# Kernel tuning notes

Measured on AMD Instinct MI355X. Metric: run time of the kernel, lower is better.

The kernel has to match this reference:

```python
import jax, jax.numpy as jnp
import numpy as np

N, F_IN, H1, NHEADS, H2, H3 = 4096, 512, 128, 4, 256, 64
ALPHA = 0.2
NEG = -9e15


def setup_inputs() -> dict:
    key = jax.random.key(0)
    k_x, k_adj, k_watt, k_a, k_w1, k_w2 = jax.random.split(key, 6)
    x = jax.random.normal(k_x, (N, F_IN), dtype=jnp.float32)
    adj = (jax.random.uniform(k_adj, (N, N)) < 0.004).astype(jnp.float32)
    adj = adj.at[jnp.arange(N), jnp.arange(N)].set(1.0)
    # xavier-ish init scales
    W_att = jax.random.normal(k_watt, (NHEADS, F_IN, H1), dtype=jnp.float32) * (1.0 / np.sqrt(F_IN))
    a = jax.random.normal(k_a, (NHEADS, 2 * H1), dtype=jnp.float32) * 0.1
    W1 = jax.random.normal(k_w1, (NHEADS * H1, H2), dtype=jnp.float32) * (1.0 / np.sqrt(NHEADS * H1))
    W2 = jax.random.normal(k_w2, (H2, H3), dtype=jnp.float32) * (1.0 / np.sqrt(H2))
    return {"x": x, "adj": adj, "W_att": W_att, "a": a, "W1": W1, "W2": W2}


def reference(x, adj, W_att, a, W1, W2):
    h1 = W_att.shape[-1]
    # --- multi-head GAT (dense masked attention, faithful to source) ---
    Wh = jnp.einsum('nf,hfo->hno', x, W_att)              # [H, N, h1]
    a1, a2 = a[:, :h1], a[:, h1:]                          # each [H, h1]
    s1 = jnp.einsum('hno,ho->hn', Wh, a1)                  # [H, N]
    s2 = jnp.einsum('hno,ho->hn', Wh, a2)                  # [H, N]
    e = jax.nn.leaky_relu(s1[:, :, None] + s2[:, None, :], ALPHA)  # [H, N, N]
    att = jax.nn.softmax(jnp.where(adj[None] > 0, e, NEG), axis=-1)
    h = jnp.einsum('hnm,hmo->hno', att, Wh)                # [H, N, h1]
    xcat = jnp.transpose(h, (1, 0, 2)).reshape(x.shape[0], -1)  # [N, H*h1]
    xr = jax.nn.relu(xcat)
    # --- GCN layers: support = x @ W; out = adj @ support ---
    g1 = jax.nn.relu(adj @ (xr @ W1))                      # [N, H2]
    g2 = adj @ (g1 @ W2)                                   # [N, H3]
    return g2, jax.nn.softmax(g2, axis=1)
```

## Files before the change

kernel.cpp:

```cpp
#include <hip/hip_runtime.h>
#include <hip/hip_bf16.h>

#define NN    4096
#define FIN   512
#define NH1   128
#define NH    4
#define NH2   256
#define NH3   64
#define CAP   64
#define ALPHA 0.2f

typedef float f32x4 __attribute__((ext_vector_type(4)));
typedef __bf16 bf16x8 __attribute__((ext_vector_type(8)));

__device__ __forceinline__ unsigned short f2bf(float f) {
    union { float f; unsigned u; } x; x.f = f;
    unsigned r = x.u + 0x7fff + ((x.u >> 16) & 1);
    return (unsigned short)(r >> 16);
}
__device__ __forceinline__ float bf2f(ushort u) {
    union { unsigned u; float f; } x; x.u = ((unsigned)u) << 16;
    return x.f;
}
__device__ __forceinline__ float bflo(unsigned w) {
    union { unsigned u; float f; } x; x.u = w << 16; return x.f;
}
__device__ __forceinline__ float bfhi(unsigned w) {
    union { unsigned u; float f; } x; x.u = w & 0xffff0000u; return x.f;
}

#define C_X     2048
#define C_WATT  (C_X + 1024)
#define C_W1T   (C_WATT + 512)
#define C_W2B   (C_W1T + 16)
#define C_Z     (C_W2B + 32)

__global__ __launch_bounds__(256) void k_conv(
    const float* __restrict__ x, ushort* __restrict__ xb,
    const float* __restrict__ W_att, ushort* __restrict__ Wattb,
    const float* __restrict__ W1, ushort* __restrict__ W1t,
    const float* __restrict__ W2, ushort* __restrict__ W2b,
    float* __restrict__ s1s2) {
    int bid = blockIdx.x;
    int tid = threadIdx.x;
    if (bid < C_X) {
        int i = (bid * 256 + tid) * 4;
        float4 v = *reinterpret_cast<const float4*>(x + i);
        ushort4 o;
        o.x = f2bf(v.x); o.y = f2bf(v.y); o.z = f2bf(v.z); o.w = f2bf(v.w);
        *reinterpret_cast<ushort4*>(xb + i) = o;
    } else if (bid < C_WATT) {
        int idx = (bid - C_X) * 256 + tid;
        int col = idx >> 9, f = idx & 511;
        int h = col >> 7, o = col & 127;
        Wattb[idx] = f2bf(W_att[h * (FIN * NH1) + f * NH1 + o]);
    } else if (bid < C_W1T) {
        int idx = (bid - C_WATT) * 256 + tid;
        int c = idx >> 9, r = idx & 511;
        W1t[idx] = f2bf(W1[(size_t)r * NH2 + c]);
    } else if (bid < C_W2B) {
        int i = ((bid - C_W1T) * 256 + tid) * 4;
        float4 v = *reinterpret_cast<const float4*>(W2 + i);
        ushort4 o;
        o.x = f2bf(v.x); o.y = f2bf(v.y); o.z = f2bf(v.z); o.w = f2bf(v.w);
        *reinterpret_cast<ushort4*>(W2b + i) = o;
    } else {
        int i = (bid - C_W2B) * 256 + tid;
        f32x4 z = {0.f, 0.f, 0.f, 0.f};
        *reinterpret_cast<f32x4*>(s1s2 + i * 4) = z;
    }
}

template <int SCORES, int MT, int BYBITS>
__global__ __launch_bounds__(256) void k_gemm(const ushort* __restrict__ A,
                                              const ushort* __restrict__ Bt,
                                              ushort* __restrict__ Cb,
                                              const float* __restrict__ av,
                                              float* __restrict__ s1,
                                              float* __restrict__ s2,
                                              int M, int N, int K) {
    __shared__ ushort As[2][32 * MT * 64];
    __shared__ ushort Bs[2][64 * 64];
    const int tid = threadIdx.x;
    const int wid = tid >> 6;
    const int lane = tid & 63;
    const int bid = blockIdx.x;
    const int row0 = (bid & ((1 << BYBITS) - 1)) * (32 * MT);
    const int col0 = (bid >> BYBITS) * 64;
    const int wr = wid >> 1, wc = wid & 1;

    f32x4 acc[MT][2] = {};
    const int nt = K / 64;

    auto stage = [&](int buf, int k0) {
        #pragma unroll
        for (int j = 0; j < MT; ++j) {
            int ci = j * 256 + tid;
            int r = ci >> 3;
            int sc = (ci & 7) ^ (r & 7);
            const ushort* ga = A + (size_t)(row0 + r) * K + k0 + sc * 8;
            ushort* la = &As[buf][(size_t)ci * 8];
            __builtin_amdgcn_global_load_lds(
                (const __attribute__((address_space(1))) unsigned int*)ga,
                (__attribute__((address_space(3))) unsigned int*)la, 16, 0, 0);
        }
        #pragma unroll
        for (int j = 0; j < 2; ++j) {
            int ci = j * 256 + tid;
            int r = ci >> 3;
            int sc = (ci & 7) ^ (r & 7);
            const ushort* gb = Bt + (size_t)(col0 + r) * K + k0 + sc * 8;
            ushort* lb = &Bs[buf][(size_t)ci * 8];
            __builtin_amdgcn_global_load_lds(
                (const __attribute__((address_space(1))) unsigned int*)gb,
                (__attribute__((address_space(3))) unsigned int*)lb, 16, 0, 0);
        }
    };

    stage(0, 0);
    __syncthreads();
    int cur = 0;
    for (int t = 0; t < nt; ++t) {
        if (t + 1 < nt) stage(cur ^ 1, (t + 1) * 64);
        #pragma unroll
        for (int kk = 0; kk < 2; ++kk) {
            bf16x8 af[MT], bfv[2];
            #pragma unroll
            for (int m = 0; m < MT; ++m) {
                int r = wr * (16 * MT) + m * 16 + (lane & 15);
                int kc = kk * 4 + (lane >> 4);
                int off = r * 64 + (((kc ^ (r & 7)) & 7) << 3);
                af[m] = *reinterpret_cast<const bf16x8*>(&As[cur][off]);
            }
            #pragma unroll
            for (int n = 0; n < 2; ++n) {
                int c = wc * 32 + n * 16 + (lane & 15);
                int kc = kk * 4 + (lane >> 4);
                int off = c * 64 + (((kc ^ (c & 7)) & 7) << 3);
                bfv[n] = *reinterpret_cast<const bf16x8*>(&Bs[cur][off]);
            }
            #pragma unroll
            for (int m = 0; m < MT; ++m)
                #pragma unroll
                for (int n = 0; n < 2; ++n)
                    acc[m][n] = __builtin_amdgcn_mfma_f32_16x16x32_bf16(af[m], bfv[n], acc[m][n], 0, 0, 0);
        }
        __syncthreads();
        cur ^= 1;
    }
    #pragma unroll
    for (int m = 0; m < MT; ++m)
        #pragma unroll
        for (int n = 0; n < 2; ++n) {
            int col = col0 + wc * 32 + n * 16 + (lane & 15);
            #pragma unroll
            for (int j2 = 0; j2 < 4; ++j2) {
                int row = row0 + wr * (16 * MT) + m * 16 + (lane >> 4) * 4 + j2;
                Cb[(size_t)row * N + col] = f2bf(acc[m][n][j2]);
            }
        }
    if (SCORES) {
        int h = col0 >> 7;
        float a1v[2], a2v[2];
        #pragma unroll
        for (int n = 0; n < 2; ++n) {
            int colh = (col0 & 127) + wc * 32 + n * 16 + (lane & 15);
            a1v[n] = av[h * 256 + colh];
            a2v[n] = av[h * 256 + 128 + colh];
        }
        #pragma unroll
        for (int m = 0; m < MT; ++m)
            #pragma unroll
            for (int j2 = 0; j2 < 4; ++j2) {
                float v1 = acc[m][0][j2] * a1v[0] + acc[m][1][j2] * a1v[1];
                float v2 = acc[m][0][j2] * a2v[0] + acc[m][1][j2] * a2v[1];
                #pragma unroll
                for (int off = 1; off < 16; off <<= 1) {
                    v1 += __shfl_xor(v1, off);
                    v2 += __shfl_xor(v2, off);
                }
                if ((lane & 15) == 0) {
                    int row = row0 + wr * (16 * MT) + m * 16 + (lane >> 4) * 4 + j2;
                    atomicAdd(&s1[h * NN + row], v1);
                    atomicAdd(&s2[h * NN + row], v2);
                }
            }
    }
}

__global__ __launch_bounds__(256) void k_attn_csr(const float* __restrict__ adj,
                                                  const ushort* __restrict__ Whb,
                                                  const float* __restrict__ s1,
                                                  const float* __restrict__ s2,
                                                  int* __restrict__ nbr,
                                                  int* __restrict__ cnt,
                                                  ushort* __restrict__ xrb) {
    __shared__ int lds_list[4][64];
    __shared__ int lds_cnt[4];
    __shared__ int mlist[CAP];
    __shared__ int stot;
    int n = blockIdx.x;
    int tid = threadIdx.x;
    int wid = tid >> 6;
    int lane = tid & 63;

    const uint4* arow = (const uint4*)(adj + (size_t)n * NN);
    uint4 v[4];
    #pragma unroll
    for (int it = 0; it < 4; ++it) v[it] = arow[wid * 256 + it * 64 + lane];
    const unsigned long long below = (1ull << lane) - 1ull;
    int base = 0;
    #pragma unroll
    for (int it = 0; it < 4; ++it) {
        unsigned long long b0 = __ballot(v[it].x != 0u);
        unsigned long long b1 = __ballot(v[it].y != 0u);
        unsigned long long b2 = __ballot(v[it].z != 0u);
        unsigned long long b3 = __ballot(v[it].w != 0u);
        int pre = __popcll(b0 & below) + __popcll(b1 & below) +
                  __popcll(b2 & below) + __popcll(b3 & below);
        int col0 = wid * 1024 + it * 256 + lane * 4;
        int pos = base + pre;
        if (v[it].x != 0u) { if (pos < 64) lds_list[wid][pos] = col0;     ++pos; }
        if (v[it].y != 0u) { if (pos < 64) lds_list[wid][pos] = col0 + 1; ++pos; }
        if (v[it].z != 0u) { if (pos < 64) lds_list[wid][pos] = col0 + 2; ++pos; }
        if (v[it].w != 0u) { if (pos < 64) lds_list[wid][pos] = col0 + 3; ++pos; }
        base += __popcll(b0) + __popcll(b1) + __popcll(b2) + __popcll(b3);
    }
    if (lane == 0) lds_cnt[wid] = base;
    __syncthreads();
    int c0 = lds_cnt[0], c1 = lds_cnt[1], c2 = lds_cnt[2], c3 = lds_cnt[3];
    {
        int off = (wid > 0 ? c0 : 0) + (wid > 1 ? c1 : 0) + (wid > 2 ? c2 : 0);
        int my = lds_cnt[wid]; if (my > 64) my = 64;
        if (lane < my) {
            int gpos = off + lane;
            if (gpos < CAP) {
                mlist[gpos] = lds_list[wid][lane];
                nbr[n * CAP + gpos] = lds_list[wid][lane];
            }
        }
        if (tid == 0) {
            int tot = c0 + c1 + c2 + c3;
            stot = tot < CAP ? tot : CAP;
            cnt[n] = stot;
        }
    }
    __syncthreads();
    int c = stot;

    int h = wid;
    int m = mlist[lane < c ? lane : 0];
    float e = -1e30f;
    float s1n = s1[h * NN + n];
    if (lane < c) {
        float t = s1n + s2[h * NN + m];
        e = (t >= 0.0f) ? t : ALPHA * t;
    }
    float mx = e;
    #pragma unroll
    for (int off = 32; off; off >>= 1) mx = fmaxf(mx, __shfl_xor(mx, off));
    float p = (lane < c) ? __expf(e - mx) : 0.0f;
    float s = p;
    #pragma unroll
    for (int off = 32; off; off >>= 1) s += __shfl_xor(s, off);
    p /= s;
    const ushort* wb = Whb + h * 128 + 2 * lane;
    float acc0 = 0.0f, acc1 = 0.0f;
    int cp8 = (c + 7) & ~7;
    for (int j = 0; j < cp8; j += 8) {
        float pj[8]; int mj[8]; unsigned wj[8];
        #pragma unroll
        for (int u = 0; u < 8; ++u) {
            pj[u] = __shfl(p, j + u);
            mj[u] = __shfl(m, j + u);
        }
        #pragma unroll
        for (int u = 0; u < 8; ++u)
            wj[u] = *reinterpret_cast<const unsigned*>(wb + (size_t)mj[u] * 512);
        #pragma unroll
        for (int u = 0; u < 8; ++u) {
            acc0 = fmaf(pj[u], bflo(wj[u]), acc0);
            acc1 = fmaf(pj[u], bfhi(wj[u]), acc1);
        }
    }
    unsigned ow = (unsigned)f2bf(fmaxf(acc0, 0.0f)) | ((unsigned)f2bf(fmaxf(acc1, 0.0f)) << 16);
    *reinterpret_cast<unsigned*>(xrb + (size_t)n * 512 + h * 128 + 2 * lane) = ow;
}

__global__ __launch_bounds__(256) void k_g1y2(const ushort* __restrict__ y1b,
                                              const int* __restrict__ nbr,
                                              const int* __restrict__ cnt,
                                              const ushort* __restrict__ W2b,
                                              float* __restrict__ y2) {
    __shared__ float g1s[2][NH2];
    __shared__ float part[2][2][NH3];
    int half = threadIdx.x >> 7;
    int t = threadIdx.x & 127;
    int n = blockIdx.x * 2 + half;
    int c = cnt[n];
    const int* nb = nbr + n * CAP;
    {
        float acc0 = 0.0f, acc1 = 0.0f;
        const ushort* yb = y1b + 2 * t;
        for (int j = 0; j < c; j += 8) {
            int idx[8]; float f[8]; unsigned w[8];
            #pragma unroll
            for (int u = 0; u < 8; ++u) {
                idx[u] = nb[(j + u < c) ? j + u : j];
                f[u] = (j + u < c) ? 1.f : 0.f;
            }
            #pragma unroll
            for (int u = 0; u < 8; ++u)
                w[u] = *reinterpret_cast<const unsigned*>(yb + (size_t)idx[u] * NH2);
            #pragma unroll
            for (int u = 0; u < 8; ++u) {
                acc0 = fmaf(f[u], bflo(w[u]), acc0);
                acc1 = fmaf(f[u], bfhi(w[u]), acc1);
            }
        }
        g1s[half][2 * t]     = fmaxf(acc0, 0.0f);
        g1s[half][2 * t + 1] = fmaxf(acc1, 0.0f);
    }
    __syncthreads();
    int q = t >> 6, col = t & 63;
    float acc = 0.0f;
    #pragma unroll 8
    for (int i = 0; i < 128; ++i) {
        int k = q * 128 + i;
        acc = fmaf(g1s[half][k], bf2f(W2b[k * NH3 + col]), acc);
    }
    part[half][q][col] = acc;
    __syncthreads();
    if (t < 64)
        y2[(size_t)n * NH3 + t] = part[half][0][t] + part[half][1][t];
}

__global__ __launch_bounds__(256) void k_final(const float* __restrict__ Y2,
                                               const int* __restrict__ nbr,
                                               const int* __restrict__ cnt,
                                               float* __restrict__ out) {
    int n = blockIdx.x * 4 + (threadIdx.x >> 6);
    int lane = threadIdx.x & 63;
    int c = cnt[n];
    const int* nb = nbr + n * CAP;
    float acc = 0.0f;
    for (int j = 0; j < c; j += 8) {
        int idx[8]; float f[8]; float v[8];
        #pragma unroll
        for (int u = 0; u < 8; ++u) {
            idx[u] = nb[(j + u < c) ? j + u : j];
            f[u] = (j + u < c) ? 1.f : 0.f;
        }
        #pragma unroll
        for (int u = 0; u < 8; ++u)
            v[u] = Y2[(size_t)idx[u] * NH3 + lane];
        #pragma unroll
        for (int u = 0; u < 8; ++u)
            acc = fmaf(f[u], v[u], acc);
    }
    out[(size_t)n * NH3 + lane] = acc;
    float mx = acc;
    #pragma unroll
    for (int off = 32; off; off >>= 1) mx = fmaxf(mx, __shfl_xor(mx, off));
    float p = __expf(acc - mx);
    float s = p;
    #pragma unroll
    for (int off = 32; off; off >>= 1) s += __shfl_xor(s, off);
    out[(size_t)NN * NH3 + (size_t)n * NH3 + lane] = p / s;
}

extern "C" void kernel_launch(void* const* d_in, const int* in_sizes, int n_in,
                              void* d_out, int out_size, void* d_ws, size_t ws_size,
                              hipStream_t stream) {
    const float* x     = (const float*)d_in[0];
    const float* adj   = (const float*)d_in[1];
    const float* W_att = (const float*)d_in[2];
    const float* a     = (const float*)d_in[3];
    const float* W1    = (const float*)d_in[4];
    const float* W2    = (const float*)d_in[5];
    float* out = (float*)d_out;

    char* p = (char*)d_ws;
    ushort* xb    = (ushort*)p; p += (size_t)NN * FIN * 2;
    ushort* Wattb = (ushort*)p; p += (size_t)FIN * NH * NH1 * 2;
    ushort* W1t   = (ushort*)p; p += (size_t)NH2 * (NH * NH1) * 2;
    ushort* W2b   = (ushort*)p; p += (size_t)NH2 * NH3 * 2;
    ushort* Whb   = (ushort*)p; p += (size_t)NN * NH * NH1 * 2;
    float*  s1    = (float*)p;  p += (size_t)NH * NN * 4;
    float*  s2    = (float*)p;  p += (size_t)NH * NN * 4;
    int*    nbr   = (int*)p;    p += (size_t)NN * CAP * 4;
    int*    cnt   = (int*)p;    p += (size_t)NN * 4;
    ushort* xrb   = (ushort*)p; p += (size_t)NN * NH * NH1 * 2;
    ushort* y1b   = (ushort*)p; p += (size_t)NN * NH2 * 2;
    float*  y2    = (float*)p;  p += (size_t)NN * NH3 * 4;

    k_conv<<<C_Z, 256, 0, stream>>>(x, xb, W_att, Wattb, W1, W1t, W2, W2b, s1);
    k_gemm<1, 2, 6><<<512, 256, 0, stream>>>(
        xb, Wattb, Whb, a, s1, s2, NN, NH * NH1, FIN);
    k_attn_csr<<<NN, 256, 0, stream>>>(adj, Whb, s1, s2, nbr, cnt, xrb);
    k_gemm<0, 1, 7><<<512, 256, 0, stream>>>(
        xrb, W1t, y1b, nullptr, nullptr, nullptr, NN, NH2, NH * NH1);
    k_g1y2<<<NN / 2, 256, 0, stream>>>(y1b, nbr, cnt, W2b, y2);
    k_final<<<NN / 4, 256, 0, stream>>>(y2, nbr, cnt, out);
}
```

Before: 66.21 us.

## Reassociate second GCN layer and move weight conversion into attention kernel

Computes adj@(g1@W2) as (adj@g1)@W2. The neighbor aggregation now runs on the 256-wide g1 (stored as bf16), and the 256x64 projection is fused into the final kernel together with the softmax. The W1/W2 bf16 conversions move from the first conversion kernel into extra blocks of the attention launch, so they no longer sit in front of the first GEMM. In exchange, the second gather is wider (256 bf16 instead of 64 fp32 per neighbor), g1 is rounded to bf16 before aggregation, and only two of four waves do the projection.

```diff
diff --git a/kernel.cpp b/kernel.cpp
--- a/kernel.cpp
+++ b/kernel.cpp
@@ -30,16 +30,14 @@
 }
 
 #define C_X     2048
+#define C_WATT  (C_X + 512)
+#undef C_WATT
 #define C_WATT  (C_X + 1024)
-#define C_W1T   (C_WATT + 512)
-#define C_W2B   (C_W1T + 16)
-#define C_Z     (C_W2B + 32)
+#define C_Z     (C_WATT + 32)
 
 __global__ __launch_bounds__(256) void k_conv(
     const float* __restrict__ x, ushort* __restrict__ xb,
     const float* __restrict__ W_att, ushort* __restrict__ Wattb,
-    const float* __restrict__ W1, ushort* __restrict__ W1t,
-    const float* __restrict__ W2, ushort* __restrict__ W2b,
     float* __restrict__ s1s2) {
     int bid = blockIdx.x;
     int tid = threadIdx.x;
@@ -54,18 +52,8 @@
         int col = idx >> 9, f = idx & 511;
         int h = col >> 7, o = col & 127;
         Wattb[idx] = f2bf(W_att[h * (FIN * NH1) + f * NH1 + o]);
-    } else if (bid < C_W1T) {
-        int idx = (bid - C_WATT) * 256 + tid;
-        int c = idx >> 9, r = idx & 511;
-        W1t[idx] = f2bf(W1[(size_t)r * NH2 + c]);
-    } else if (bid < C_W2B) {
-        int i = ((bid - C_W1T) * 256 + tid) * 4;
-        float4 v = *reinterpret_cast<const float4*>(W2 + i);
-        ushort4 o;
-        o.x = f2bf(v.x); o.y = f2bf(v.y); o.z = f2bf(v.z); o.w = f2bf(v.w);
-        *reinterpret_cast<ushort4*>(W2b + i) = o;
     } else {
-        int i = (bid - C_W2B) * 256 + tid;
+        int i = (bid - C_WATT) * 256 + tid;
         f32x4 z = {0.f, 0.f, 0.f, 0.f};
         *reinterpret_cast<f32x4*>(s1s2 + i * 4) = z;
     }
@@ -188,19 +176,42 @@
     }
 }
 
+#define ATT_N   4096
+#define ATT_W1  (ATT_N + 512)
+#define ATT_W2  (ATT_W1 + 16)
+
 __global__ __launch_bounds__(256) void k_attn_csr(const float* __restrict__ adj,
                                                   const ushort* __restrict__ Whb,
                                                   const float* __restrict__ s1,
                                                   const float* __restrict__ s2,
                                                   int* __restrict__ nbr,
                                                   int* __restrict__ cnt,
-                                                  ushort* __restrict__ xrb) {
+                                                  ushort* __restrict__ xrb,
+                                                  const float* __restrict__ W1,
+                                                  ushort* __restrict__ W1t,
+                                                  const float* __restrict__ W2,
+                                                  ushort* __restrict__ W2b) {
+    int tid = threadIdx.x;
+    if (blockIdx.x >= ATT_N) {
+        int bid = blockIdx.x;
+        if (bid < ATT_W1) {
+            int idx = (bid - ATT_N) * 256 + tid;
+            int c = idx >> 9, r = idx & 511;
+            W1t[idx] = f2bf(W1[(size_t)r * NH2 + c]);
+        } else {
+            int i = ((bid - ATT_W1) * 256 + tid) * 4;
+            float4 v = *reinterpret_cast<const float4*>(W2 + i);
+            ushort4 o;
+            o.x = f2bf(v.x); o.y = f2bf(v.y); o.z = f2bf(v.z); o.w = f2bf(v.w);
+            *reinterpret_cast<ushort4*>(W2b + i) = o;
+        }
+        return;
+    }
     __shared__ int lds_list[4][64];
     __shared__ int lds_cnt[4];
     __shared__ int mlist[CAP];
     __shared__ int stot;
     int n = blockIdx.x;
-    int tid = threadIdx.x;
     int wid = tid >> 6;
     int lane = tid & 63;
 
@@ -287,21 +298,52 @@
     *reinterpret_cast<unsigned*>(xrb + (size_t)n * 512 + h * 128 + 2 * lane) = ow;
 }
 
-__global__ __launch_bounds__(256) void k_g1y2(const ushort* __restrict__ y1b,
-                                              const int* __restrict__ nbr,
-                                              const int* __restrict__ cnt,
-                                              const ushort* __restrict__ W2b,
-                                              float* __restrict__ y2) {
-    __shared__ float g1s[2][NH2];
-    __shared__ float part[2][2][NH3];
+__global__ __launch_bounds__(256) void k_g1(const ushort* __restrict__ y1b,
+                                            const int* __restrict__ nbr,
+                                            const int* __restrict__ cnt,
+                                            ushort* __restrict__ g1b) {
     int half = threadIdx.x >> 7;
     int t = threadIdx.x & 127;
     int n = blockIdx.x * 2 + half;
     int c = cnt[n];
     const int* nb = nbr + n * CAP;
+    float acc0 = 0.0f, acc1 = 0.0f;
+    const ushort* yb = y1b + 2 * t;
+    for (int j = 0; j < c; j += 8) {
+        int idx[8]; float f[8]; unsigned w[8];
+        #pragma unroll
+        for (int u = 0; u < 8; ++u) {
+            idx[u] = nb[(j + u < c) ? j + u : j];
+            f[u] = (j + u < c) ? 1.f : 0.f;
+        }
+        #pragma unroll
+        for (int u = 0; u < 8; ++u)
+            w[u] = *reinterpret_cast<const unsigned*>(yb + (size_t)idx[u] * NH2);
+        #pragma unroll
+        for (int u = 0; u < 8; ++u) {
+            acc0 = fmaf(f[u], bflo(w[u]), acc0);
+            acc1 = fmaf(f[u], bfhi(w[u]), acc1);
+        }
+    }
+    unsigned ow = (unsigned)f2bf(fmaxf(acc0, 0.0f)) | ((unsigned)f2bf(fmaxf(acc1, 0.0f)) << 16);
+    *reinterpret_cast<unsigned*>(g1b + (size_t)n * NH2 + 2 * t) = ow;
+}
+
+__global__ __launch_bounds__(256) void k_final2(const ushort* __restrict__ g1b,
+                                                const int* __restrict__ nbr,
+                                                const int* __restrict__ cnt,
+                                                const ushort* __restrict__ W2b,
+                                                float* __restrict__ out) {
+    __shared__ float h2s[2][NH2];
+    int half = threadIdx.x >> 7;
+    int t = threadIdx.x & 127;
+    int n0 = blockIdx.x * 2;
     {
+        int n = n0 + half;
+        int c = cnt[n];
+        const int* nb = nbr + n * CAP;
         float acc0 = 0.0f, acc1 = 0.0f;
-        const ushort* yb = y1b + 2 * t;
+        const ushort* gb = g1b + 2 * t;
         for (int j = 0; j < c; j += 8) {
             int idx[8]; float f[8]; unsigned w[8];
             #pragma unroll
@@ -311,62 +353,36 @@
             }
             #pragma unroll
             for (int u = 0; u < 8; ++u)
-                w[u] = *reinterpret_cast<const unsigned*>(yb + (size_t)idx[u] * NH2);
+                w[u] = *reinterpret_cast<const unsigned*>(gb + (size_t)idx[u] * NH2);
             #pragma unroll
             for (int u = 0; u < 8; ++u) {
                 acc0 = fmaf(f[u], bflo(w[u]), acc0);
                 acc1 = fmaf(f[u], bfhi(w[u]), acc1);
             }
         }
-        g1s[half][2 * t]     = fmaxf(acc0, 0.0f);
-        g1s[half][2 * t + 1] = fmaxf(acc1, 0.0f);
+        h2s[half][2 * t]     = acc0;
+        h2s[half][2 * t + 1] = acc1;
     }
     __syncthreads();
-    int q = t >> 6, col = t & 63;
-    float acc = 0.0f;
-    #pragma unroll 8
-    for (int i = 0; i < 128; ++i) {
-        int k = q * 128 + i;
-        acc = fmaf(g1s[half][k], bf2f(W2b[k * NH3 + col]), acc);
-    }
-    part[half][q][col] = acc;
-    __syncthreads();
-    if (t < 64)
-        y2[(size_t)n * NH3 + t] = part[half][0][t] + part[half][1][t];
-}
-
-__global__ __launch_bounds__(256) void k_final(const float* __restrict__ Y2,
-                                               const int* __restrict__ nbr,
-                                               const int* __restrict__ cnt,
-                                               float* __restrict__ out) {
-    int n = blockIdx.x * 4 + (threadIdx.x >> 6);
+    int wid = threadIdx.x >> 6;
     int lane = threadIdx.x & 63;
-    int c = cnt[n];
-    const int* nb = nbr + n * CAP;
-    float acc = 0.0f;
-    for (int j = 0; j < c; j += 8) {
-        int idx[8]; float f[8]; float v[8];
-        #pragma unroll
-        for (int u = 0; u < 8; ++u) {
-            idx[u] = nb[(j + u < c) ? j + u : j];
-            f[u] = (j + u < c) ? 1.f : 0.f;
-        }
-        #pragma unroll
-        for (int u = 0; u < 8; ++u)
-            v[u] = Y2[(size_t)idx[u] * NH3 + lane];
-        #pragma unroll
-        for (int u = 0; u < 8; ++u)
-            acc = fmaf(f[u], v[u], acc);
-    }
-    out[(size_t)n * NH3 + lane] = acc;
-    float mx = acc;
-    #pragma unroll
-    for (int off = 32; off; off >>= 1) mx = fmaxf(mx, __shfl_xor(mx, off));
-    float p = __expf(acc - mx);
-    float s = p;
-    #pragma unroll
-    for (int off = 32; off; off >>= 1) s += __shfl_xor(s, off);
-    out[(size_t)NN * NH3 + (size_t)n * NH3 + lane] = p / s;
+    if (wid < 2) {
+        int n = n0 + wid;
+        const float* h2 = h2s[wid];
+        float acc = 0.0f;
+        #pragma unroll 8
+        for (int k = 0; k < NH2; ++k)
+            acc = fmaf(h2[k], bf2f(W2b[k * NH3 + lane]), acc);
+        out[(size_t)n * NH3 + lane] = acc;
+        float mx = acc;
+        #pragma unroll
+        for (int off = 32; off; off >>= 1) mx = fmaxf(mx, __shfl_xor(mx, off));
+        float p = __expf(acc - mx);
+        float s = p;
+        #pragma unroll
+        for (int off = 32; off; off >>= 1) s += __shfl_xor(s, off);
+        out[(size_t)NN * NH3 + (size_t)n * NH3 + lane] = p / s;
+    }
 }
 
 extern "C" void kernel_launch(void* const* d_in, const int* in_sizes, int n_in,
@@ -392,14 +408,15 @@
     int*    cnt   = (int*)p;    p += (size_t)NN * 4;
     ushort* xrb   = (ushort*)p; p += (size_t)NN * NH * NH1 * 2;
     ushort* y1b   = (ushort*)p; p += (size_t)NN * NH2 * 2;
-    float*  y2    = (float*)p;  p += (size_t)NN * NH3 * 4;
-
-    k_conv<<<C_Z, 256, 0, stream>>>(x, xb, W_att, Wattb, W1, W1t, W2, W2b, s1);
+    ushort* g1b   = (ushort*)p; p += (size_t)NN * NH2 * 2;
+
+    k_conv<<<C_Z, 256, 0, stream>>>(x, xb, W_att, Wattb, s1);
     k_gemm<1, 2, 6><<<512, 256, 0, stream>>>(
         xb, Wattb, Whb, a, s1, s2, NN, NH * NH1, FIN);
-    k_attn_csr<<<NN, 256, 0, stream>>>(adj, Whb, s1, s2, nbr, cnt, xrb);
+    k_attn_csr<<<ATT_W2, 256, 0, stream>>>(adj, Whb, s1, s2, nbr, cnt, xrb,
+                                           W1, W1t, W2, W2b);
     k_gemm<0, 1, 7><<<512, 256, 0, stream>>>(
         xrb, W1t, y1b, nullptr, nullptr, nullptr, NN, NH2, NH * NH1);
-    k_g1y2<<<NN / 2, 256, 0, stream>>>(y1b, nbr, cnt, W2b, y2);
-    k_final<<<NN / 4, 256, 0, stream>>>(y2, nbr, cnt, out);
-}
+    k_g1<<<NN / 2, 256, 0, stream>>>(y1b, nbr, cnt, g1b);
+    k_final2<<<NN / 2, 256, 0, stream>>>(g1b, nbr, cnt, W2b, out);
+}
```

New measurement: 67.88 us. +2.5%, slower.
